# Optimization experiments

Hardware: AMD Instinct MI355X
Metric: run time of the kernel (lower is better)

The kernel has to match this reference:

```python
import jax, jax.numpy as jnp
import numpy as np

E = 256      # embed_dim
H = 4        # num_heads
EXP = 4      # expansion_factor
B, C, R = 8, 32, 255  # batch, max_cols, rows (seq = R+1 with CLS)
LN_EPS = 1e-5


def setup_inputs() -> dict:
    key = jax.random.key(0)
    ks = jax.random.split(key, 16)
    s = 0.02
    return {
        "x": jax.random.normal(ks[0], (B, C, R, E), jnp.float32),
        "real_cols": jax.random.randint(ks[1], (B,), 0, C + 1),
        "real_rows": jax.random.randint(ks[2], (B,), 0, R + 1),
        "cls_token": jax.random.normal(ks[3], (E,), jnp.float32) * s,
        # MHA in_proj (torch packs q,k,v as (3E, E)) and out_proj
        "w_qkv": jax.random.normal(ks[4], (3 * E, E), jnp.float32) * s,
        "b_qkv": jnp.zeros((3 * E,), jnp.float32),
        "w_out": jax.random.normal(ks[5], (E, E), jnp.float32) * s,
        "b_out": jnp.zeros((E,), jnp.float32),
        # LayerNorm
        "ln_g": jnp.ones((E,), jnp.float32),
        "ln_b": jnp.zeros((E,), jnp.float32),
        # FFN: Linear(E, 4E) -> ReLU -> Linear(4E, E)
        "w1": jax.random.normal(ks[6], (EXP * E, E), jnp.float32) * s,
        "b1": jnp.zeros((EXP * E,), jnp.float32),
        "w2": jax.random.normal(ks[7], (E, EXP * E), jnp.float32) * s,
        "b2": jnp.zeros((E,), jnp.float32),
    }


def reference(x, real_cols, real_rows, cls_token, w_qkv, b_qkv, w_out, b_out,
              ln_g, ln_b, w1, b1, w2, b2):
    Bn, Cn, Rn, En = x.shape
    S = Rn + 1
    Dh = En // H
    dt = x.dtype

    # prepend CLS token to every column's row sequence -> (B, C, S, E)
    cls = jnp.broadcast_to(cls_token.astype(dt), (Bn, Cn, 1, En))
    xc = jnp.concatenate([cls, x], axis=2)

    # fused qkv projection
    qkv = jnp.einsum('bcse,fe->bcsf', xc, w_qkv.astype(dt)) + b_qkv.astype(dt)
    q, k, v = jnp.split(qkv, 3, axis=-1)
    q = q.reshape(Bn, Cn, S, H, Dh)
    k = k.reshape(Bn, Cn, S, H, Dh)
    v = v.reshape(Bn, Cn, S, H, Dh)

    scale = 1.0 / np.sqrt(Dh).astype(np.float32)
    scores = jnp.einsum('bcqhd,bckhd->bchqk', q, k) * scale  # (B,C,H,S,S)

    # key_padding_mask: position 0 (CLS) always valid; row p (1..R) valid iff p <= nrow
    pos = jnp.arange(S)
    valid = (pos[None, :] == 0) | (pos[None, :] <= real_rows[:, None])  # (B, S)
    neg = jnp.asarray(-1e9, scores.dtype)
    scores = jnp.where(valid[:, None, None, None, :], scores, neg)

    attn = jax.nn.softmax(scores, axis=-1)
    ctx = jnp.einsum('bchqk,bckhd->bcqhd', attn, v).reshape(Bn, Cn, S, En)
    mha = jnp.einsum('bcse,fe->bcsf', ctx, w_out.astype(dt)) + b_out.astype(dt)

    # LayerNorm over E
    mu = mha.mean(axis=-1, keepdims=True)
    var = ((mha - mu) ** 2).mean(axis=-1, keepdims=True)
    ln = (mha - mu) * jax.lax.rsqrt(var + LN_EPS) * ln_g.astype(dt) + ln_b.astype(dt)

    # FFN with residual from ln (out = ln + ffn(ln))
    h = jax.nn.relu(jnp.einsum('bcse,fe->bcsf', ln, w1.astype(dt)) + b1.astype(dt))
    ffn = jnp.einsum('bcsf,ef->bcse', h, w2.astype(dt)) + b2.astype(dt)
    out = ln + ffn

    # rep_mode == 'cls': take CLS position; zero out padded columns
    rep = out[:, :, 0, :]  # (B, C, E)
    col_valid = (jnp.arange(Cn)[None, :] < real_cols[:, None]).astype(dt)
    return rep * col_valid[..., None]
```

## Files before the change

kernel.cpp:

```cpp
#include <hip/hip_runtime.h>
#include <math.h>

static constexpr int kC = 32, kR = 255, kE = 256;

__device__ float g_q0kv[768];
__device__ float g_qw[4 * 256];
__device__ float g_s0[4];
__device__ float g_qb[4];
__device__ float g_m[256 * 4 * 4];
__device__ float g_l[256 * 4 * 4];
__device__ float g_part[256 * 4 * 4 * 256];
__device__ float g_ln[256 * 256];
__device__ float g_hact[256 * 1024];

__global__ __launch_bounds__(256) void k_setup1(const float* __restrict__ cls,
                                                const float* __restrict__ w_qkv,
                                                const float* __restrict__ b_qkv) {
  const int t = threadIdx.x, wv = t >> 6, l = t & 63;
  const int row = blockIdx.x * 4 + wv;
  float4 wv4 = *(const float4*)(w_qkv + (size_t)row * 256 + 4 * l);
  float4 cv4 = *(const float4*)(cls + 4 * l);
  float acc = wv4.x * cv4.x + wv4.y * cv4.y + wv4.z * cv4.z + wv4.w * cv4.w;
#pragma unroll
  for (int m = 1; m < 64; m <<= 1) acc += __shfl_xor(acc, m);
  if (l == 0) g_q0kv[row] = acc + b_qkv[row];
}

__global__ __launch_bounds__(256) void k_setup2(const float* __restrict__ w_qkv,
                                                const float* __restrict__ b_qkv) {
  const int h = blockIdx.x, t = threadIdx.x;
  __shared__ float q0s[64];
  if (t < 64) q0s[t] = g_q0kv[h * 64 + t];
  __syncthreads();
  float acc = 0.f;
#pragma unroll 8
  for (int j = 0; j < 64; ++j)
    acc += q0s[j] * w_qkv[(size_t)(256 + h * 64 + j) * 256 + t];
  g_qw[h * 256 + t] = acc * 0.125f;
  if (t < 64) {
    float q = q0s[t];
    float pk = q * g_q0kv[256 + h * 64 + t];
    float pb = q * b_qkv[256 + h * 64 + t];
#pragma unroll
    for (int m = 1; m < 64; m <<= 1) {
      pk += __shfl_xor(pk, m);
      pb += __shfl_xor(pb, m);
    }
    if (t == 0) {
      g_s0[h] = pk * 0.125f;
      g_qb[h] = pb * 0.125f;
    }
  }
}

__global__ __launch_bounds__(256) void k_attn(const float* __restrict__ x,
                                              const int* __restrict__ real_cols,
                                              const int* __restrict__ real_rows) {
  const int bc = blockIdx.x, chunk = blockIdx.y;
  const int b = bc >> 5, c = bc & 31;
  if (c >= real_cols[b]) return;
  const int rr = real_rows[b];
  const int r0 = chunk * 64;
  const int nr = min(64, rr - r0);
  if (nr <= 0) return;

  __shared__ float xsT[256][65];
  __shared__ float qws[4 * 256];
  __shared__ float ps[4][64];
  const int t = threadIdx.x, wv = t >> 6, l = t & 63;

#pragma unroll
  for (int i = 0; i < 4; ++i) qws[i * 256 + t] = g_qw[i * 256 + t];

  const float* xb = x + ((size_t)bc * kR + r0) * kE;
  for (int r = wv; r < nr; r += 4) {
    float4 v = *(const float4*)(xb + (size_t)r * kE + 4 * l);
    xsT[4 * l + 0][r] = v.x;
    xsT[4 * l + 1][r] = v.y;
    xsT[4 * l + 2][r] = v.z;
    xsT[4 * l + 3][r] = v.w;
  }
  __syncthreads();

  const int h = wv, row = l;
  float acc = 0.f;
#pragma unroll 8
  for (int e = 0; e < 256; ++e) acc += qws[h * 256 + e] * xsT[e][row];
  float s = (row < nr) ? acc + g_qb[h] : -1e30f;
  float mx = s;
#pragma unroll
  for (int m = 1; m < 64; m <<= 1) mx = fmaxf(mx, __shfl_xor(mx, m));
  float p = (row < nr) ? __expf(s - mx) : 0.f;
  float lsum = p;
#pragma unroll
  for (int m = 1; m < 64; m <<= 1) lsum += __shfl_xor(lsum, m);
  ps[h][row] = p;
  if (l == 0) {
    g_m[(bc * 4 + chunk) * 4 + h] = mx;
    g_l[(bc * 4 + chunk) * 4 + h] = lsum;
  }
  __syncthreads();

  float a0 = 0.f, a1 = 0.f, a2 = 0.f, a3 = 0.f;
  for (int r2 = 0; r2 < nr; ++r2) {
    float xv = xsT[t][r2];
    a0 += ps[0][r2] * xv;
    a1 += ps[1][r2] * xv;
    a2 += ps[2][r2] * xv;
    a3 += ps[3][r2] * xv;
  }
  float* pp = g_part + (size_t)(bc * 4 + chunk) * 4 * 256;
  pp[0 * 256 + t] = a0;
  pp[1 * 256 + t] = a1;
  pp[2 * 256 + t] = a2;
  pp[3 * 256 + t] = a3;
}

__global__ __launch_bounds__(256) void k_tail1(const int* __restrict__ real_cols,
                                               const int* __restrict__ real_rows,
                                               const float* __restrict__ w_qkv,
                                               const float* __restrict__ w_out,
                                               const float* __restrict__ b_qkv,
                                               const float* __restrict__ b_out,
                                               const float* __restrict__ ln_g,
                                               const float* __restrict__ ln_b) {
  const int t = threadIdx.x;
  const int tok0 = blockIdx.x * 4;
  __shared__ float xb4[4][4][256];
  __shared__ float ctx4[4][256];
  __shared__ float mh4[4][256];
  __shared__ float al[4][4][4];
  __shared__ float p04[4][4];
  __shared__ float stats[4][2];
  __shared__ int valids[4];

  if (t < 16) {
    const int i = t >> 2, h = t & 3, bc = tok0 + i, b = bc >> 5, c = bc & 31;
    const int valid = (c < real_cols[b]);
    if (h == 0) valids[i] = valid;
    float a0 = 0.f, a1 = 0.f, a2 = 0.f, a3 = 0.f, p0 = 0.f;
    if (valid) {
      const int rr = real_rows[b];
      const int nch = (rr + 63) >> 6;
      const float s0 = g_s0[h];
      float M = s0;
      for (int ch = 0; ch < nch; ++ch) M = fmaxf(M, g_m[(bc * 4 + ch) * 4 + h]);
      float av[4] = {0.f, 0.f, 0.f, 0.f};
      float lt = __expf(s0 - M);
      const float w0 = lt;
      for (int ch = 0; ch < nch; ++ch) {
        float e = __expf(g_m[(bc * 4 + ch) * 4 + h] - M);
        av[ch] = e;
        lt += g_l[(bc * 4 + ch) * 4 + h] * e;
      }
      const float inv = 1.f / lt;
      a0 = av[0] * inv; a1 = av[1] * inv; a2 = av[2] * inv; a3 = av[3] * inv;
      p0 = w0 * inv;
    }
    al[i][h][0] = a0; al[i][h][1] = a1; al[i][h][2] = a2; al[i][h][3] = a3;
    p04[i][h] = p0;
  }
  __syncthreads();

#pragma unroll
  for (int i = 0; i < 4; ++i) {
    const int bc = tok0 + i;
#pragma unroll
    for (int h = 0; h < 4; ++h) {
      const float* pp = g_part + (size_t)bc * 4 * 4 * 256 + h * 256 + t;
      float a = al[i][h][0] * pp[0] + al[i][h][1] * pp[4 * 256] +
                al[i][h][2] * pp[8 * 256] + al[i][h][3] * pp[12 * 256];
      xb4[i][h][t] = a;
    }
  }
  __syncthreads();

  {
    const int h = t >> 6;
    const float* wrow = w_qkv + (size_t)(512 + t) * 256;
    const float vc = g_q0kv[512 + t];
    const float bv = b_qkv[512 + t];
    float acc[4];
#pragma unroll
    for (int i = 0; i < 4; ++i) acc[i] = p04[i][h] * vc + (1.f - p04[i][h]) * bv;
    for (int e = 0; e < 256; e += 4) {
      float4 w4 = *(const float4*)(wrow + e);
#pragma unroll
      for (int i = 0; i < 4; ++i)
        acc[i] += w4.x * xb4[i][h][e] + w4.y * xb4[i][h][e + 1] +
                  w4.z * xb4[i][h][e + 2] + w4.w * xb4[i][h][e + 3];
    }
#pragma unroll
    for (int i = 0; i < 4; ++i) ctx4[i][t] = acc[i];
  }
  __syncthreads();

  {
    const float* wrow = w_out + (size_t)t * 256;
    const float bo = b_out[t];
    float acc[4];
#pragma unroll
    for (int i = 0; i < 4; ++i) acc[i] = bo;
    for (int e = 0; e < 256; e += 4) {
      float4 w4 = *(const float4*)(wrow + e);
#pragma unroll
      for (int i = 0; i < 4; ++i)
        acc[i] += w4.x * ctx4[i][e] + w4.y * ctx4[i][e + 1] +
                  w4.z * ctx4[i][e + 2] + w4.w * ctx4[i][e + 3];
    }
#pragma unroll
    for (int i = 0; i < 4; ++i) mh4[i][t] = acc[i];
  }
  __syncthreads();

  {
    const int i = t >> 6, l = t & 63;
    float s1 = 0.f, s2 = 0.f;
#pragma unroll
    for (int k = 0; k < 4; ++k) {
      float v = mh4[i][l + 64 * k];
      s1 += v;
      s2 += v * v;
    }
#pragma unroll
    for (int m = 1; m < 64; m <<= 1) {
      s1 += __shfl_xor(s1, m);
      s2 += __shfl_xor(s2, m);
    }
    if (l == 0) {
      float mu = s1 * (1.f / 256.f);
      float var = s2 * (1.f / 256.f) - mu * mu;
      stats[i][0] = mu;
      stats[i][1] = rsqrtf(var + 1e-5f);
    }
  }
  __syncthreads();
  const float lg = ln_g[t], lb = ln_b[t];
#pragma unroll
  for (int i = 0; i < 4; ++i)
    g_ln[(size_t)(tok0 + i) * 256 + t] =
        (mh4[i][t] - stats[i][0]) * stats[i][1] * lg + lb;
}

__global__ __launch_bounds__(256) void k_ffn1(const float* __restrict__ w1,
                                              const float* __restrict__ b1) {
  __shared__ float lns[8][256];
  const int t = threadIdx.x;
  const int tok0 = blockIdx.x * 8, f0 = blockIdx.y * 128;
#pragma unroll
  for (int i = 0; i < 8; ++i) lns[i][t] = g_ln[(size_t)(tok0 + i) * 256 + t];
  __syncthreads();
  const int f = f0 + (t & 127), half = t >> 7;
  const float* wrow = w1 + (size_t)f * 256;
  const float bb = b1[f];
  float acc[4] = {bb, bb, bb, bb};
  for (int e = 0; e < 256; e += 4) {
    float4 w4 = *(const float4*)(wrow + e);
#pragma unroll
    for (int k = 0; k < 4; ++k) {
      const int i = half * 4 + k;
      acc[k] += w4.x * lns[i][e] + w4.y * lns[i][e + 1] +
                w4.z * lns[i][e + 2] + w4.w * lns[i][e + 3];
    }
  }
#pragma unroll
  for (int k = 0; k < 4; ++k)
    g_hact[(size_t)(tok0 + half * 4 + k) * 1024 + f] = fmaxf(acc[k], 0.f);
}

__global__ __launch_bounds__(256) void k_ffn2(const float* __restrict__ w2,
                                              const float* __restrict__ b2,
                                              const int* __restrict__ real_cols,
                                              float* __restrict__ out) {
  __shared__ float hs[8][1024];
  const int t = threadIdx.x;
  const int tok0 = blockIdx.x * 8, e0 = blockIdx.y * 32;
#pragma unroll
  for (int i = 0; i < 8; ++i) {
#pragma unroll
    for (int j = 0; j < 4; ++j)
      hs[i][j * 256 + t] = g_hact[(size_t)(tok0 + i) * 1024 + j * 256 + t];
  }
  __syncthreads();
  const int e = e0 + (t & 31), i = t >> 5;
  const int tok = tok0 + i, b = tok >> 5, c = tok & 31;
  const float* wrow = w2 + (size_t)e * 1024;
  float acc = b2[e];
  for (int f = 0; f < 1024; f += 4) {
    float4 w4 = *(const float4*)(wrow + f);
    acc += w4.x * hs[i][f] + w4.y * hs[i][f + 1] + w4.z * hs[i][f + 2] +
           w4.w * hs[i][f + 3];
  }
  const float lnv = g_ln[(size_t)tok * 256 + e];
  out[(size_t)tok * 256 + e] = (c < real_cols[b]) ? (lnv + acc) : 0.f;
}

extern "C" void kernel_launch(void* const* d_in, const int* in_sizes, int n_in,
                              void* d_out, int out_size, void* d_ws, size_t ws_size,
                              hipStream_t stream) {
  const float* x = (const float*)d_in[0];
  const int* real_cols = (const int*)d_in[1];
  const int* real_rows = (const int*)d_in[2];
  const float* cls = (const float*)d_in[3];
  const float* w_qkv = (const float*)d_in[4];
  const float* b_qkv = (const float*)d_in[5];
  const float* w_out = (const float*)d_in[6];
  const float* b_out = (const float*)d_in[7];
  const float* ln_g = (const float*)d_in[8];
  const float* ln_b = (const float*)d_in[9];
  const float* w1 = (const float*)d_in[10];
  const float* b1 = (const float*)d_in[11];
  const float* w2 = (const float*)d_in[12];
  const float* b2 = (const float*)d_in[13];
  float* out = (float*)d_out;
  (void)in_sizes; (void)n_in; (void)out_size; (void)d_ws; (void)ws_size;

  k_setup1<<<192, 256, 0, stream>>>(cls, w_qkv, b_qkv);
  k_setup2<<<4, 256, 0, stream>>>(w_qkv, b_qkv);
  k_attn<<<dim3(256, 4), 256, 0, stream>>>(x, real_cols, real_rows);
  k_tail1<<<64, 256, 0, stream>>>(real_cols, real_rows, w_qkv, w_out, b_qkv,
                                  b_out, ln_g, ln_b);
  k_ffn1<<<dim3(32, 8), 256, 0, stream>>>(w1, b1);
  k_ffn2<<<dim3(32, 8), 256, 0, stream>>>(w2, b2, real_cols, out);
}
```

Before: 190.5 us.

## Skip padded columns in tail/FFN kernels and untranspose attention x tile

The attention kernel now stores x rows in shared memory untransposed with padding and computes the scores with float4 dot products, replacing the scalar transposed scatter. The tail kernel runs one token per block across 256 blocks, skips invalid columns, and only reads the partial chunks that exist. The FFN kernels exit early for 8-token groups that contain only padded columns, and ffn2 writes zeros for those. This cuts wasted work on padding and raises parallelism, at the cost of less weight reuse per block in the tail.

After: 195.5 us. +2.6%, slower.

```diff
diff --git a/kernel.cpp b/kernel.cpp
--- a/kernel.cpp
+++ b/kernel.cpp
@@ -64,28 +64,29 @@
   const int nr = min(64, rr - r0);
   if (nr <= 0) return;
 
-  __shared__ float xsT[256][65];
-  __shared__ float qws[4 * 256];
+  __shared__ float xs[64][260];
+  __shared__ float qws[4][256];
   __shared__ float ps[4][64];
   const int t = threadIdx.x, wv = t >> 6, l = t & 63;
 
 #pragma unroll
-  for (int i = 0; i < 4; ++i) qws[i * 256 + t] = g_qw[i * 256 + t];
+  for (int i = 0; i < 4; ++i) qws[i][t] = g_qw[i * 256 + t];
 
   const float* xb = x + ((size_t)bc * kR + r0) * kE;
-  for (int r = wv; r < nr; r += 4) {
-    float4 v = *(const float4*)(xb + (size_t)r * kE + 4 * l);
-    xsT[4 * l + 0][r] = v.x;
-    xsT[4 * l + 1][r] = v.y;
-    xsT[4 * l + 2][r] = v.z;
-    xsT[4 * l + 3][r] = v.w;
-  }
+  for (int r = wv; r < nr; r += 4)
+    *(float4*)&xs[r][4 * l] = *(const float4*)(xb + (size_t)r * kE + 4 * l);
   __syncthreads();
 
   const int h = wv, row = l;
   float acc = 0.f;
+  const float4* qrow = (const float4*)&qws[h][0];
+  const float4* xrow = (const float4*)&xs[row][0];
 #pragma unroll 8
-  for (int e = 0; e < 256; ++e) acc += qws[h * 256 + e] * xsT[e][row];
+  for (int e4 = 0; e4 < 64; ++e4) {
+    float4 q4 = qrow[e4];
+    float4 x4 = xrow[e4];
+    acc += q4.x * x4.x + q4.y * x4.y + q4.z * x4.z + q4.w * x4.w;
+  }
   float s = (row < nr) ? acc + g_qb[h] : -1e30f;
   float mx = s;
 #pragma unroll
@@ -103,7 +104,7 @@
 
   float a0 = 0.f, a1 = 0.f, a2 = 0.f, a3 = 0.f;
   for (int r2 = 0; r2 < nr; ++r2) {
-    float xv = xsT[t][r2];
+    float xv = xs[r2][t];
     a0 += ps[0][r2] * xv;
     a1 += ps[1][r2] * xv;
     a2 += ps[2][r2] * xv;
@@ -116,137 +117,112 @@
   pp[3 * 256 + t] = a3;
 }
 
-__global__ __launch_bounds__(256) void k_tail1(const int* __restrict__ real_cols,
-                                               const int* __restrict__ real_rows,
-                                               const float* __restrict__ w_qkv,
-                                               const float* __restrict__ w_out,
-                                               const float* __restrict__ b_qkv,
-                                               const float* __restrict__ b_out,
-                                               const float* __restrict__ ln_g,
-                                               const float* __restrict__ ln_b) {
-  const int t = threadIdx.x;
-  const int tok0 = blockIdx.x * 4;
-  __shared__ float xb4[4][4][256];
-  __shared__ float ctx4[4][256];
-  __shared__ float mh4[4][256];
-  __shared__ float al[4][4][4];
-  __shared__ float p04[4][4];
-  __shared__ float stats[4][2];
-  __shared__ int valids[4];
-
-  if (t < 16) {
-    const int i = t >> 2, h = t & 3, bc = tok0 + i, b = bc >> 5, c = bc & 31;
-    const int valid = (c < real_cols[b]);
-    if (h == 0) valids[i] = valid;
-    float a0 = 0.f, a1 = 0.f, a2 = 0.f, a3 = 0.f, p0 = 0.f;
-    if (valid) {
-      const int rr = real_rows[b];
-      const int nch = (rr + 63) >> 6;
-      const float s0 = g_s0[h];
-      float M = s0;
-      for (int ch = 0; ch < nch; ++ch) M = fmaxf(M, g_m[(bc * 4 + ch) * 4 + h]);
-      float av[4] = {0.f, 0.f, 0.f, 0.f};
-      float lt = __expf(s0 - M);
-      const float w0 = lt;
-      for (int ch = 0; ch < nch; ++ch) {
-        float e = __expf(g_m[(bc * 4 + ch) * 4 + h] - M);
-        av[ch] = e;
-        lt += g_l[(bc * 4 + ch) * 4 + h] * e;
-      }
-      const float inv = 1.f / lt;
-      a0 = av[0] * inv; a1 = av[1] * inv; a2 = av[2] * inv; a3 = av[3] * inv;
-      p0 = w0 * inv;
-    }
-    al[i][h][0] = a0; al[i][h][1] = a1; al[i][h][2] = a2; al[i][h][3] = a3;
-    p04[i][h] = p0;
-  }
-  __syncthreads();
-
-#pragma unroll
-  for (int i = 0; i < 4; ++i) {
-    const int bc = tok0 + i;
-#pragma unroll
-    for (int h = 0; h < 4; ++h) {
-      const float* pp = g_part + (size_t)bc * 4 * 4 * 256 + h * 256 + t;
-      float a = al[i][h][0] * pp[0] + al[i][h][1] * pp[4 * 256] +
-                al[i][h][2] * pp[8 * 256] + al[i][h][3] * pp[12 * 256];
-      xb4[i][h][t] = a;
-    }
+__global__ __launch_bounds__(256) void k_tail(const int* __restrict__ real_cols,
+                                              const int* __restrict__ real_rows,
+                                              const float* __restrict__ w_qkv,
+                                              const float* __restrict__ w_out,
+                                              const float* __restrict__ b_qkv,
+                                              const float* __restrict__ b_out,
+                                              const float* __restrict__ ln_g,
+                                              const float* __restrict__ ln_b) {
+  const int bc = blockIdx.x, b = bc >> 5, c = bc & 31;
+  if (c >= real_cols[b]) return;
+  const int rr = real_rows[b];
+  const int nch = (rr + 63) >> 6;
+  const int t = threadIdx.x, wv = t >> 6, l = t & 63;
+
+  __shared__ float xb[4][256];
+  __shared__ float ctxs[256];
+  __shared__ float al[4][4];
+  __shared__ float p0s[4];
+  __shared__ float rb[2][4];
+
+  if (t < 4) {
+    const int h = t;
+    const float s0 = g_s0[h];
+    float M = s0;
+    for (int ch = 0; ch < nch; ++ch) M = fmaxf(M, g_m[(bc * 4 + ch) * 4 + h]);
+    float lt = __expf(s0 - M);
+    const float w0 = lt;
+    float av[4] = {0.f, 0.f, 0.f, 0.f};
+    for (int ch = 0; ch < nch; ++ch) {
+      float e = __expf(g_m[(bc * 4 + ch) * 4 + h] - M);
+      av[ch] = e;
+      lt += g_l[(bc * 4 + ch) * 4 + h] * e;
+    }
+    const float inv = 1.f / lt;
+#pragma unroll
+    for (int ch = 0; ch < 4; ++ch) al[h][ch] = av[ch] * inv;
+    p0s[h] = w0 * inv;
+  }
+  __syncthreads();
+
+#pragma unroll
+  for (int h = 0; h < 4; ++h) {
+    float a = 0.f;
+    for (int ch = 0; ch < nch; ++ch)
+      a += al[h][ch] * g_part[(size_t)(bc * 4 + ch) * 4 * 256 + h * 256 + t];
+    xb[h][t] = a;
   }
   __syncthreads();
 
   {
-    const int h = t >> 6;
+    const int h = wv;
+    const float p0 = p0s[h];
     const float* wrow = w_qkv + (size_t)(512 + t) * 256;
-    const float vc = g_q0kv[512 + t];
-    const float bv = b_qkv[512 + t];
-    float acc[4];
-#pragma unroll
-    for (int i = 0; i < 4; ++i) acc[i] = p04[i][h] * vc + (1.f - p04[i][h]) * bv;
-    for (int e = 0; e < 256; e += 4) {
-      float4 w4 = *(const float4*)(wrow + e);
-#pragma unroll
-      for (int i = 0; i < 4; ++i)
-        acc[i] += w4.x * xb4[i][h][e] + w4.y * xb4[i][h][e + 1] +
-                  w4.z * xb4[i][h][e + 2] + w4.w * xb4[i][h][e + 3];
-    }
-#pragma unroll
-    for (int i = 0; i < 4; ++i) ctx4[i][t] = acc[i];
-  }
-  __syncthreads();
-
+    float acc = p0 * g_q0kv[512 + t] + (1.f - p0) * b_qkv[512 + t];
+    const float4* v4p = (const float4*)&xb[h][0];
+#pragma unroll 8
+    for (int e4 = 0; e4 < 64; ++e4) {
+      float4 w4 = *(const float4*)(wrow + 4 * e4);
+      float4 v4 = v4p[e4];
+      acc += w4.x * v4.x + w4.y * v4.y + w4.z * v4.z + w4.w * v4.w;
+    }
+    ctxs[t] = acc;
+  }
+  __syncthreads();
+
+  float mh;
   {
     const float* wrow = w_out + (size_t)t * 256;
-    const float bo = b_out[t];
-    float acc[4];
-#pragma unroll
-    for (int i = 0; i < 4; ++i) acc[i] = bo;
-    for (int e = 0; e < 256; e += 4) {
-      float4 w4 = *(const float4*)(wrow + e);
-#pragma unroll
-      for (int i = 0; i < 4; ++i)
-        acc[i] += w4.x * ctx4[i][e] + w4.y * ctx4[i][e + 1] +
-                  w4.z * ctx4[i][e + 2] + w4.w * ctx4[i][e + 3];
-    }
-#pragma unroll
-    for (int i = 0; i < 4; ++i) mh4[i][t] = acc[i];
-  }
-  __syncthreads();
-
-  {
-    const int i = t >> 6, l = t & 63;
-    float s1 = 0.f, s2 = 0.f;
-#pragma unroll
-    for (int k = 0; k < 4; ++k) {
-      float v = mh4[i][l + 64 * k];
-      s1 += v;
-      s2 += v * v;
-    }
-#pragma unroll
-    for (int m = 1; m < 64; m <<= 1) {
-      s1 += __shfl_xor(s1, m);
-      s2 += __shfl_xor(s2, m);
-    }
-    if (l == 0) {
-      float mu = s1 * (1.f / 256.f);
-      float var = s2 * (1.f / 256.f) - mu * mu;
-      stats[i][0] = mu;
-      stats[i][1] = rsqrtf(var + 1e-5f);
-    }
-  }
-  __syncthreads();
-  const float lg = ln_g[t], lb = ln_b[t];
-#pragma unroll
-  for (int i = 0; i < 4; ++i)
-    g_ln[(size_t)(tok0 + i) * 256 + t] =
-        (mh4[i][t] - stats[i][0]) * stats[i][1] * lg + lb;
+    float acc = b_out[t];
+    const float4* c4 = (const float4*)&ctxs[0];
+#pragma unroll 8
+    for (int e4 = 0; e4 < 64; ++e4) {
+      float4 w4 = *(const float4*)(wrow + 4 * e4);
+      float4 v4 = c4[e4];
+      acc += w4.x * v4.x + w4.y * v4.y + w4.z * v4.z + w4.w * v4.w;
+    }
+    mh = acc;
+  }
+
+  float s1 = mh, s2 = mh * mh;
+#pragma unroll
+  for (int m = 1; m < 64; m <<= 1) {
+    s1 += __shfl_xor(s1, m);
+    s2 += __shfl_xor(s2, m);
+  }
+  if (l == 0) {
+    rb[0][wv] = s1;
+    rb[1][wv] = s2;
+  }
+  __syncthreads();
+  const float mu = (rb[0][0] + rb[0][1] + rb[0][2] + rb[0][3]) * (1.f / 256.f);
+  const float msq = (rb[1][0] + rb[1][1] + rb[1][2] + rb[1][3]) * (1.f / 256.f);
+  const float var = msq - mu * mu;
+  g_ln[(size_t)bc * 256 + t] =
+      (mh - mu) * rsqrtf(var + 1e-5f) * ln_g[t] + ln_b[t];
 }
 
 __global__ __launch_bounds__(256) void k_ffn1(const float* __restrict__ w1,
-                                              const float* __restrict__ b1) {
+                                              const float* __restrict__ b1,
+                                              const int* __restrict__ real_cols) {
+  const int tok0 = blockIdx.x * 8;
+  const int b = tok0 >> 5, c0 = tok0 & 31;
+  if (c0 >= real_cols[b]) return;
   __shared__ float lns[8][256];
   const int t = threadIdx.x;
-  const int tok0 = blockIdx.x * 8, f0 = blockIdx.y * 128;
+  const int f0 = blockIdx.y * 128;
 #pragma unroll
   for (int i = 0; i < 8; ++i) lns[i][t] = g_ln[(size_t)(tok0 + i) * 256 + t];
   __syncthreads();
@@ -272,9 +248,15 @@
                                               const float* __restrict__ b2,
                                               const int* __restrict__ real_cols,
                                               float* __restrict__ out) {
-  __shared__ float hs[8][1024];
   const int t = threadIdx.x;
   const int tok0 = blockIdx.x * 8, e0 = blockIdx.y * 32;
+  const int b = tok0 >> 5, c0 = tok0 & 31;
+  const int ncols = real_cols[b];
+  if (c0 >= ncols) {
+    out[(size_t)(tok0 + (t >> 5)) * 256 + e0 + (t & 31)] = 0.f;
+    return;
+  }
+  __shared__ float hs[8][1024];
 #pragma unroll
   for (int i = 0; i < 8; ++i) {
 #pragma unroll
@@ -283,7 +265,7 @@
   }
   __syncthreads();
   const int e = e0 + (t & 31), i = t >> 5;
-  const int tok = tok0 + i, b = tok >> 5, c = tok & 31;
+  const int tok = tok0 + i, c = tok & 31;
   const float* wrow = w2 + (size_t)e * 1024;
   float acc = b2[e];
   for (int f = 0; f < 1024; f += 4) {
@@ -292,7 +274,7 @@
            w4.w * hs[i][f + 3];
   }
   const float lnv = g_ln[(size_t)tok * 256 + e];
-  out[(size_t)tok * 256 + e] = (c < real_cols[b]) ? (lnv + acc) : 0.f;
+  out[(size_t)tok * 256 + e] = (c < ncols) ? (lnv + acc) : 0.f;
 }
 
 extern "C" void kernel_launch(void* const* d_in, const int* in_sizes, int n_in,
@@ -318,8 +300,8 @@
   k_setup1<<<192, 256, 0, stream>>>(cls, w_qkv, b_qkv);
   k_setup2<<<4, 256, 0, stream>>>(w_qkv, b_qkv);
   k_attn<<<dim3(256, 4), 256, 0, stream>>>(x, real_cols, real_rows);
-  k_tail1<<<64, 256, 0, stream>>>(real_cols, real_rows, w_qkv, w_out, b_qkv,
+  k_tail<<<256, 256, 0, stream>>>(real_cols, real_rows, w_qkv, w_out, b_qkv,
                                   b_out, ln_g, ln_b);
-  k_ffn1<<<dim3(32, 8), 256, 0, stream>>>(w1, b1);
+  k_ffn1<<<dim3(32, 8), 256, 0, stream>>>(w1, b1, real_cols);
   k_ffn2<<<dim3(32, 8), 256, 0, stream>>>(w2, b2, real_cols, out);
 }
```
